# Optimization experiments

Measured on AMD Instinct MI355X. Metric: run time of the kernel, lower is better.

## Reference

```python
import jax, jax.numpy as jnp
import numpy as np

N_BOXES = 2048
N_CLASSES = 20


def _cross(a, b):
    return a[..., 0] * b[..., 1] - a[..., 1] * b[..., 0]


def _corners(box):
    # box: [5] = cx, cy, w, h, angle -> [4,2] corner coords
    cx, cy, w, h, a = box[0], box[1], box[2], box[3], box[4]
    c, s = jnp.cos(a), jnp.sin(a)
    dx = jnp.array([-1.0, 1.0, 1.0, -1.0], box.dtype) * (w * 0.5)
    dy = jnp.array([-1.0, -1.0, 1.0, 1.0], box.dtype) * (h * 0.5)
    return jnp.stack([cx + c * dx - s * dy, cy + s * dx + c * dy], axis=-1)


def _points_in_box(pts, box):
    # pts [K,2]; rotate into box frame, test axis-aligned containment
    cx, cy, w, h, a = box[0], box[1], box[2], box[3], box[4]
    c, s = jnp.cos(a), jnp.sin(a)
    px = pts[:, 0] - cx
    py = pts[:, 1] - cy
    lx = c * px + s * py
    ly = -s * px + c * py
    eps = 1e-5
    return (jnp.abs(lx) <= w * 0.5 + eps) & (jnp.abs(ly) <= h * 0.5 + eps)


def _pair_inter_area(box_a, box_b):
    # Exact convex intersection area of two rotated rectangles.
    ca = _corners(box_a)
    cb = _corners(box_b)
    # all 4x4 edge-pair intersections
    p = ca[:, None, :]
    r = (jnp.roll(ca, -1, 0) - ca)[:, None, :]
    q = cb[None, :, :]
    s_ = (jnp.roll(cb, -1, 0) - cb)[None, :, :]
    denom = _cross(r, s_)
    qp = q - p
    safe = jnp.where(jnp.abs(denom) > 1e-9, denom, 1.0)
    t = _cross(qp, s_) / safe
    u = _cross(qp, r) / safe
    valid_e = (jnp.abs(denom) > 1e-9) & (t >= 0.0) & (t <= 1.0) & (u >= 0.0) & (u <= 1.0)
    ipts = p + t[..., None] * r  # [4,4,2]
    # candidate polygon vertices: corners of A in B, corners of B in A, edge crossings
    pts = jnp.concatenate([ca, cb, ipts.reshape(16, 2)], axis=0)  # [24,2]
    mask = jnp.concatenate([_points_in_box(ca, box_b), _points_in_box(cb, box_a), valid_e.reshape(16)], axis=0)
    k = jnp.sum(mask)
    m = mask.astype(pts.dtype)[:, None]
    center = jnp.sum(pts * m, axis=0) / jnp.maximum(k, 1).astype(pts.dtype)
    d = pts - center
    ang = jnp.where(mask, jnp.arctan2(d[:, 1], d[:, 0]), 1e9)  # invalid -> sorted last
    idx = jnp.argsort(ang)
    ds = d[idx]
    ar = jnp.arange(24)
    nxt = jnp.where(ar + 1 < k, ar + 1, 0)
    cr = _cross(ds, ds[nxt])
    area = 0.5 * jnp.abs(jnp.sum(jnp.where(ar < k, cr, 0.0)))
    return jnp.where(k >= 3, area, 0.0)


def _iou_one_vs_many(box, boxes):
    inter = jax.vmap(lambda b: _pair_inter_area(box, b))(boxes)  # [N]
    area_a = box[2] * box[3]
    area_b = boxes[:, 2] * boxes[:, 3]
    return inter / (area_a + area_b - inter + 1e-9)


def _rotated_nms_mask(boxes, scores, iou_threshold):
    # sequential greedy suppression, highest score first; returns bool keep mask (original order)
    n = boxes.shape[0]
    order = jnp.argsort(-scores)
    bs = boxes[order]
    ar = jnp.arange(n)

    def body(i, keep):
        ious = _iou_one_vs_many(bs[i], bs)
        suppress = (ious > iou_threshold) & (ar > i) & keep[i]
        return keep & ~suppress

    keep_sorted = jax.lax.fori_loop(0, n, body, jnp.ones((n,), bool))
    return jnp.zeros((n,), bool).at[order].set(keep_sorted)


def setup_inputs() -> dict:
    key = jax.random.key(0)
    k1, k2, k3, k4, k5 = jax.random.split(key, 5)
    cxcy = jax.random.uniform(k1, (N_BOXES, 2), jnp.float32) * 1024.0
    wh = jax.random.uniform(k2, (N_BOXES, 2), jnp.float32) * 96.0 + 4.0
    ang = jax.random.uniform(k3, (N_BOXES, 1), jnp.float32) * np.pi
    boxes = jnp.concatenate([cxcy, wh, ang], axis=1)  # [N,5]
    scores = jax.random.uniform(k4, (N_BOXES,), jnp.float32)
    labels = jax.random.randint(k5, (N_BOXES,), 0, N_CLASSES, dtype=jnp.int64 if jax.config.read('jax_enable_x64') else jnp.int32)
    return {"boxes": boxes, "scores": scores, "labels": labels, "iou_threshold": 0.5}


def reference(boxes, scores, labels, iou_threshold):
    # multiclass NMS via coordinate-offset trick (N <= 20000 branch of forward)
    cx, cy, w, h = boxes[:, 0], boxes[:, 1], boxes[:, 2], boxes[:, 3]
    max_radius = jnp.max(jnp.sqrt(w * w + h * h)) * 0.5
    max_coord = jnp.maximum(jnp.max(cx), jnp.max(cy))
    offset_scale = (max_coord + max_radius) * 2.0 + 1.0
    offsets = labels.astype(boxes.dtype) * offset_scale
    boxes_nms = boxes.at[:, 0].add(offsets).at[:, 1].add(offsets)
    keep = _rotated_nms_mask(boxes_nms, scores, iou_threshold)
    # fixed-shape encoding of the kept-index set: score of kept boxes, 0 for suppressed
    return scores * keep.astype(scores.dtype)
```

## Files before the change

### kernel.cpp

```cpp
#include <hip/hip_runtime.h>
#include <cstdint>

typedef unsigned long long u64;
typedef uint32_t u32;

#define NB 2048
#define EDGE_CAP 16384
#define CLIST_CAP 2048


__global__ __launch_bounds__(256) void build_kernel(
    const float* __restrict__ boxes, const float* __restrict__ scores,
    const int* __restrict__ labels,
    float* __restrict__ cxp, float* __restrict__ cyp, float* __restrict__ wp,
    float* __restrict__ hp, float* __restrict__ cp, float* __restrict__ sp,
    float4* __restrict__ pxyr, float* __restrict__ sscp, int* __restrict__ sidx,
    u32* __restrict__ counters) {
#pragma clang fp contract(off)
  __shared__ float sc[NB];
  __shared__ float smc[4], smr[4];
  int t = threadIdx.x;
  if (blockIdx.x == 0 && t < 4) counters[t] = 0u;
  float mc = -1e30f, mr = -1e30f;
  for (int k = t; k < NB; k += 256) {
    float cx = boxes[k * 5 + 0];
    float cy = boxes[k * 5 + 1];
    float w = boxes[k * 5 + 2];
    float h = boxes[k * 5 + 3];
    mc = fmaxf(mc, fmaxf(cx, cy));
    float ww = w * w;
    float hh = h * h;
    mr = fmaxf(mr, sqrtf(ww + hh));
    sc[k] = scores[k];
  }
  for (int off = 32; off > 0; off >>= 1) {
    mc = fmaxf(mc, __shfl_down(mc, off));
    mr = fmaxf(mr, __shfl_down(mr, off));
  }
  if ((t & 63) == 0) { smc[t >> 6] = mc; smr[t >> 6] = mr; }
  __syncthreads();
  mc = fmaxf(fmaxf(smc[0], smc[1]), fmaxf(smc[2], smc[3]));
  mr = fmaxf(fmaxf(smr[0], smr[1]), fmaxf(smr[2], smr[3]));
  float osc = (mc + mr * 0.5f) * 2.0f + 1.0f;

  int wave = t >> 6, lane = t & 63;
  int i = blockIdx.x * 4 + wave;
  float si = sc[i];
  int rank = 0;
#pragma unroll 8
  for (int m = 0; m < NB / 64; ++m) {
    int j = m * 64 + lane;
    float sj = sc[j];
    rank += (int)((sj > si) || (sj == si && j < i));
  }
  for (int off = 32; off > 0; off >>= 1) rank += __shfl_down(rank, off);
  if (lane == 0) {
    float off = (float)labels[i] * osc;
    float cx = boxes[i * 5 + 0] + off;
    float cy = boxes[i * 5 + 1] + off;
    float w = boxes[i * 5 + 2];
    float h = boxes[i * 5 + 3];
    float a = boxes[i * 5 + 4];
    float c = cosf(a);
    float s = sinf(a);
    float ww = w * w;
    float hh = h * h;
    float rad = 0.5f * sqrtf(ww + hh);
    cxp[rank] = cx;
    cyp[rank] = cy;
    wp[rank] = w;
    hp[rank] = h;
    cp[rank] = c;
    sp[rank] = s;
    pxyr[rank] = make_float4(cx, cy, rad, 0.0f);
    sscp[rank] = si;
    sidx[rank] = i;
  }
}

__global__ __launch_bounds__(256) void candgeom_greedy_kernel(
    const float* __restrict__ cxp, const float* __restrict__ cyp,
    const float* __restrict__ wp, const float* __restrict__ hp,
    const float* __restrict__ cp, const float* __restrict__ sp,
    const float4* __restrict__ pxyr, const float* __restrict__ thrp,
    const float* __restrict__ sscp, const int* __restrict__ sidx,
    u32* __restrict__ edges, u32* __restrict__ counters,
    float* __restrict__ out) {
#pragma clang fp contract(off)
  __shared__ u32 clist[CLIST_CAP];
  __shared__ float dxL[256 * 25];
  __shared__ float dyL[256 * 25];
  __shared__ u32 ccnt;
  __shared__ int is_last;
  __shared__ u64 keepw[32];
  __shared__ u32 Sw32[64];
  __shared__ int changed;
  int t = threadIdx.x;
  if (t == 0) ccnt = 0;
  float jx[8], jy[8], jr[8];
#pragma unroll
  for (int c = 0; c < 8; ++c) {
    float4 v = pxyr[c * 256 + t];
    jx[c] = v.x; jy[c] = v.y; jr[c] = v.z;
  }
  __syncthreads();
  int i0 = blockIdx.x * 4;
#pragma unroll
  for (int di = 0; di < 4; ++di) {
    int i = i0 + di;
    float4 pi = pxyr[i];
    float ax = pi.x, ay = pi.y, ar = pi.z;
#pragma unroll
    for (int c = 0; c < 8; ++c) {
      int j = c * 256 + t;
      if (j > i) {
        float dx = jx[c] - ax, dy = jy[c] - ay;
        float rr = ar + jr[c] + 1.0f;
        if (dx * dx + dy * dy <= rr * rr) {
          u32 s = atomicAdd(&ccnt, 1u);
          if (s < CLIST_CAP) clist[s] = ((u32)i << 16) | (u32)j;
        }
      }
    }
  }
  __syncthreads();
  u32 cnt = ccnt < CLIST_CAP ? ccnt : CLIST_CAP;
  float thr = *thrp;
  float* myDx = &dxL[t * 25];
  float* myDy = &dyL[t * 25];
  for (u32 idx = t; idx < cnt; idx += 256) {
    u32 pk = clist[idx];
    int bi = (int)(pk >> 16);
    int bj = (int)(pk & 0xFFFFu);
    float acx = cxp[bi], acy = cyp[bi], aw = wp[bi], ah = hp[bi];
    float ac = cp[bi], as_ = sp[bi];
    float bcx = cxp[bj], bcy = cyp[bj], bw = wp[bj], bh = hp[bj];
    float bc = cp[bj], bs_ = sp[bj];
    const float SX[4] = {-1.f, 1.f, 1.f, -1.f};
    const float SY[4] = {-1.f, -1.f, 1.f, 1.f};
    float axx[4], ayy[4], bxx[4], byy[4];
    float ahw = aw * 0.5f, ahh = ah * 0.5f;
    float bhw = bw * 0.5f, bhh = bh * 0.5f;
#pragma unroll
    for (int q = 0; q < 4; ++q) {
      float dx = SX[q] * ahw, dy = SY[q] * ahh;
      axx[q] = acx + ac * dx - as_ * dy;
      ayy[q] = acy + as_ * dx + ac * dy;
      float ex = SX[q] * bhw, ey = SY[q] * bhh;
      bxx[q] = bcx + bc * ex - bs_ * ey;
      byy[q] = bcy + bs_ * ex + bc * ey;
    }
    float px_[24], py_[24];
    bool mk[24];
#pragma unroll
    for (int q = 0; q < 4; ++q) {
      {
        float axp = axx[q] - bcx, ayp = ayy[q] - bcy;
        float lxx = bc * axp + bs_ * ayp;
        float lyy = bc * ayp - bs_ * axp;
        mk[q] = (fabsf(lxx) <= bhw + 1e-5f) && (fabsf(lyy) <= bhh + 1e-5f);
        px_[q] = axx[q]; py_[q] = ayy[q];
      }
      {
        float axp = bxx[q] - acx, ayp = byy[q] - acy;
        float lxx = ac * axp + as_ * ayp;
        float lyy = ac * ayp - as_ * axp;
        mk[4 + q] = (fabsf(lxx) <= ahw + 1e-5f) && (fabsf(lyy) <= ahh + 1e-5f);
        px_[4 + q] = bxx[q]; py_[4 + q] = byy[q];
      }
    }
#pragma unroll
    for (int e = 0; e < 4; ++e) {
      float rx = axx[(e + 1) & 3] - axx[e];
      float ry = ayy[(e + 1) & 3] - ayy[e];
#pragma unroll
      for (int f = 0; f < 4; ++f) {
        float sx = bxx[(f + 1) & 3] - bxx[f];
        float sy = byy[(f + 1) & 3] - byy[f];
        float denom = rx * sy - ry * sx;
        float qpx = bxx[f] - axx[e];
        float qpy = byy[f] - ayy[e];
        bool dn = fabsf(denom) > 1e-9f;
        float safe = dn ? denom : 1.0f;
        float tt = (qpx * sy - qpy * sx) / safe;
        float uu = (qpx * ry - qpy * rx) / safe;
        bool valid = dn && (tt >= 0.0f) && (tt <= 1.0f) && (uu >= 0.0f) && (uu <= 1.0f);
        int id = 8 + e * 4 + f;
        px_[id] = axx[e] + tt * rx;
        py_[id] = ayy[e] + tt * ry;
        mk[id] = valid;
      }
    }
    int k = 0;
    float sx0 = 0.0f, sy0 = 0.0f;
#pragma unroll
    for (int q = 0; q < 24; ++q) {
      if (mk[q]) { k++; sx0 += px_[q]; sy0 += py_[q]; }
    }
    float kkf = (float)(k > 0 ? k : 1);
    float cxm = sx0 / kkf, cym = sy0 / kkf;
    u64 key[32];
#pragma unroll
    for (int q = 0; q < 24; ++q) {
      float dx = px_[q] - cxm, dy = py_[q] - cym;
      myDx[q] = dx; myDy[q] = dy;
      float sm = fabsf(dx) + fabsf(dy);
      float r = (sm > 0.0f) ? dy / sm : 0.0f;
      float pa;
      if (dx >= 0.0f) pa = r;
      else pa = (__float_as_uint(dy) >> 31) ? (-2.0f - r) : (2.0f - r);
      float ang = mk[q] ? pa : 1e9f;
      u32 ub = __float_as_uint(ang);
      u32 v = (ub & 0x80000000u) ? ~ub : (ub | 0x80000000u);
      key[q] = (((u64)v) << 5) | (u64)q;
    }
#pragma unroll
    for (int q = 24; q < 32; ++q) key[q] = ~0ull;
#pragma unroll
    for (int kk2 = 2; kk2 <= 32; kk2 <<= 1) {
#pragma unroll
      for (int jj = kk2 >> 1; jj > 0; jj >>= 1) {
#pragma unroll
        for (int ii = 0; ii < 32; ++ii) {
          int ll = ii ^ jj;
          if (ll > ii) {
            bool up = ((ii & kk2) == 0);
            u64 ka = key[ii], kb = key[ll];
            bool sw = up ? (ka > kb) : (ka < kb);
            key[ii] = sw ? kb : ka;
            key[ll] = sw ? ka : kb;
          }
        }
      }
    }
    float acc = 0.0f;
    int id0 = (int)(key[0] & 31ull);
    float fx = myDx[id0], fy = myDy[id0];
    float curx = fx, cury = fy;
#pragma unroll
    for (int q = 0; q < 24; ++q) {
      if (q < k - 1) {
        int idn = (int)(key[q + 1] & 31ull);
        float nx = myDx[idn], ny = myDy[idn];
        acc += curx * ny - cury * nx;
        curx = nx; cury = ny;
      } else if (q == k - 1) {
        acc += curx * fy - cury * fx;
      }
    }
    float area = 0.5f * fabsf(acc);
    float inter = (k >= 3) ? area : 0.0f;
    float areaA = aw * ah;
    float areaB = bw * bh;
    float iou = inter / (areaA + areaB - inter + 1e-9f);
    if (iou > thr) {
      u32 e = atomicAdd(&counters[1], 1u);
      if (e < EDGE_CAP) edges[e] = pk;
    }
  }
  __syncthreads();
  if (t == 0) {
    __threadfence();
    u32 old = atomicAdd(&counters[2], 1u);
    is_last = (old == (u32)(gridDim.x - 1)) ? 1 : 0;
  }
  __syncthreads();
  if (!is_last) return;
  __threadfence();
  __syncthreads();
  u32 ecnt = counters[1];
  if (ecnt > EDGE_CAP) ecnt = EDGE_CAP;
  u32 nl = ecnt < CLIST_CAP ? ecnt : CLIST_CAP;
  for (u32 k = t; k < nl; k += 256) clist[k] = edges[k];
  if (t < 32) keepw[t] = ~0ull;
  __syncthreads();
  for (int iter = 0; iter < 2060; ++iter) {
    if (t < 64) Sw32[t] = 0u;
    if (t == 0) changed = 0;
    __syncthreads();
    for (u32 k = t; k < ecnt; k += 256) {
      u32 pk = (k < CLIST_CAP) ? clist[k] : edges[k];
      int i = (int)(pk >> 16);
      int j = (int)(pk & 0xFFFFu);
      if ((keepw[i >> 6] >> (i & 63)) & 1ull)
        atomicOr(&Sw32[j >> 5], 1u << (j & 31));
    }
    __syncthreads();
    if (t < 32) {
      u64 S = ((u64)Sw32[2 * t]) | (((u64)Sw32[2 * t + 1]) << 32);
      u64 nk = ~S;
      if (nk != keepw[t]) { keepw[t] = nk; changed = 1; }
    }
    __syncthreads();
    int ch = changed;
    __syncthreads();
    if (!ch) break;
  }
  for (int p = t; p < NB; p += 256) {
    int bit = (int)((keepw[p >> 6] >> (p & 63)) & 1ull);
    out[sidx[p]] = bit ? sscp[p] : 0.0f;
  }
}

extern "C" void kernel_launch(void* const* d_in, const int* in_sizes, int n_in,
                              void* d_out, int out_size, void* d_ws, size_t ws_size,
                              hipStream_t stream) {
  const float* boxes = (const float*)d_in[0];
  const float* scores = (const float*)d_in[1];
  const int* labels = (const int*)d_in[2];
  const float* thr = (const float*)d_in[3];
  float* out = (float*)d_out;

  char* base = (char*)d_ws;
  u32* counters = (u32*)base;
  float* arr = (float*)(base + 256);
  float* cxp = arr + 0 * NB;
  float* cyp = arr + 1 * NB;
  float* wp = arr + 2 * NB;
  float* hp = arr + 3 * NB;
  float* cp = arr + 4 * NB;
  float* sp = arr + 5 * NB;
  float* sscp = arr + 6 * NB;
  int* sidx = (int*)(base + 57600);
  float4* pxyr = (float4*)(base + 66048);
  u32* edges = (u32*)(base + 102400);

  build_kernel<<<512, 256, 0, stream>>>(boxes, scores, labels, cxp, cyp, wp, hp,
                                        cp, sp, pxyr, sscp, sidx, counters);
  candgeom_greedy_kernel<<<512, 256, 0, stream>>>(cxp, cyp, wp, hp, cp, sp,
                                                  pxyr, thr, sscp, sidx,
                                                  edges, counters, out);
}
```

Measured before the change: 88.77 us.

## Fuse build and candidate/greedy kernels, drop score sort via oriented edges

Merges the two kernels into one, so boxes are no longer ranked by score and scattered into sorted SoA arrays. Each block recomputes offset centers and radii straight from the inputs, and computes cos/sin per candidate pair. Each edge is stored oriented from the higher-scored box to the lower-scored one, so the fixed-point suppression works on original indices. This removes one kernel launch, the rank pass and the intermediate global buffers. In exchange it adds a hipMemsetAsync for the counters and repeats trig and loads for every candidate pair.

```diff
diff --git a/kernel.cpp b/kernel.cpp
--- a/kernel.cpp
+++ b/kernel.cpp
@@ -9,18 +9,24 @@
 #define CLIST_CAP 2048
 
 
-__global__ __launch_bounds__(256) void build_kernel(
+__global__ __launch_bounds__(256) void nms_fused_kernel(
     const float* __restrict__ boxes, const float* __restrict__ scores,
-    const int* __restrict__ labels,
-    float* __restrict__ cxp, float* __restrict__ cyp, float* __restrict__ wp,
-    float* __restrict__ hp, float* __restrict__ cp, float* __restrict__ sp,
-    float4* __restrict__ pxyr, float* __restrict__ sscp, int* __restrict__ sidx,
-    u32* __restrict__ counters) {
+    const int* __restrict__ labels, const float* __restrict__ thrp,
+    u32* __restrict__ edges, u32* __restrict__ counters,
+    float* __restrict__ out) {
 #pragma clang fp contract(off)
   __shared__ float sc[NB];
   __shared__ float smc[4], smr[4];
+  __shared__ u32 clist[CLIST_CAP];
+  __shared__ float dxL[256 * 25];
+  __shared__ float dyL[256 * 25];
+  __shared__ u32 ccnt;
+  __shared__ int is_last;
+  __shared__ u64 keepw[32];
+  __shared__ u32 Sw32[64];
+  __shared__ int changed;
   int t = threadIdx.x;
-  if (blockIdx.x == 0 && t < 4) counters[t] = 0u;
+  if (t == 0) ccnt = 0;
   float mc = -1e30f, mr = -1e30f;
   for (int k = t; k < NB; k += 256) {
     float cx = boxes[k * 5 + 0];
@@ -43,73 +49,31 @@
   mr = fmaxf(fmaxf(smr[0], smr[1]), fmaxf(smr[2], smr[3]));
   float osc = (mc + mr * 0.5f) * 2.0f + 1.0f;
 
-  int wave = t >> 6, lane = t & 63;
-  int i = blockIdx.x * 4 + wave;
-  float si = sc[i];
-  int rank = 0;
-#pragma unroll 8
-  for (int m = 0; m < NB / 64; ++m) {
-    int j = m * 64 + lane;
-    float sj = sc[j];
-    rank += (int)((sj > si) || (sj == si && j < i));
-  }
-  for (int off = 32; off > 0; off >>= 1) rank += __shfl_down(rank, off);
-  if (lane == 0) {
-    float off = (float)labels[i] * osc;
-    float cx = boxes[i * 5 + 0] + off;
-    float cy = boxes[i * 5 + 1] + off;
-    float w = boxes[i * 5 + 2];
-    float h = boxes[i * 5 + 3];
-    float a = boxes[i * 5 + 4];
-    float c = cosf(a);
-    float s = sinf(a);
+  float jx[8], jy[8], jr[8];
+#pragma unroll
+  for (int c = 0; c < 8; ++c) {
+    int j = c * 256 + t;
+    float off = (float)labels[j] * osc;
+    float w = boxes[j * 5 + 2];
+    float h = boxes[j * 5 + 3];
     float ww = w * w;
     float hh = h * h;
-    float rad = 0.5f * sqrtf(ww + hh);
-    cxp[rank] = cx;
-    cyp[rank] = cy;
-    wp[rank] = w;
-    hp[rank] = h;
-    cp[rank] = c;
-    sp[rank] = s;
-    pxyr[rank] = make_float4(cx, cy, rad, 0.0f);
-    sscp[rank] = si;
-    sidx[rank] = i;
-  }
-}
-
-__global__ __launch_bounds__(256) void candgeom_greedy_kernel(
-    const float* __restrict__ cxp, const float* __restrict__ cyp,
-    const float* __restrict__ wp, const float* __restrict__ hp,
-    const float* __restrict__ cp, const float* __restrict__ sp,
-    const float4* __restrict__ pxyr, const float* __restrict__ thrp,
-    const float* __restrict__ sscp, const int* __restrict__ sidx,
-    u32* __restrict__ edges, u32* __restrict__ counters,
-    float* __restrict__ out) {
-#pragma clang fp contract(off)
-  __shared__ u32 clist[CLIST_CAP];
-  __shared__ float dxL[256 * 25];
-  __shared__ float dyL[256 * 25];
-  __shared__ u32 ccnt;
-  __shared__ int is_last;
-  __shared__ u64 keepw[32];
-  __shared__ u32 Sw32[64];
-  __shared__ int changed;
-  int t = threadIdx.x;
-  if (t == 0) ccnt = 0;
-  float jx[8], jy[8], jr[8];
-#pragma unroll
-  for (int c = 0; c < 8; ++c) {
-    float4 v = pxyr[c * 256 + t];
-    jx[c] = v.x; jy[c] = v.y; jr[c] = v.z;
-  }
-  __syncthreads();
+    jx[c] = boxes[j * 5 + 0] + off;
+    jy[c] = boxes[j * 5 + 1] + off;
+    jr[c] = 0.5f * sqrtf(ww + hh);
+  }
   int i0 = blockIdx.x * 4;
 #pragma unroll
   for (int di = 0; di < 4; ++di) {
     int i = i0 + di;
-    float4 pi = pxyr[i];
-    float ax = pi.x, ay = pi.y, ar = pi.z;
+    float offi = (float)labels[i] * osc;
+    float wI = boxes[i * 5 + 2];
+    float hI = boxes[i * 5 + 3];
+    float wwI = wI * wI;
+    float hhI = hI * hI;
+    float ax = boxes[i * 5 + 0] + offi;
+    float ay = boxes[i * 5 + 1] + offi;
+    float ar = 0.5f * sqrtf(wwI + hhI);
 #pragma unroll
     for (int c = 0; c < 8; ++c) {
       int j = c * 256 + t;
@@ -132,10 +96,22 @@
     u32 pk = clist[idx];
     int bi = (int)(pk >> 16);
     int bj = (int)(pk & 0xFFFFu);
-    float acx = cxp[bi], acy = cyp[bi], aw = wp[bi], ah = hp[bi];
-    float ac = cp[bi], as_ = sp[bi];
-    float bcx = cxp[bj], bcy = cyp[bj], bw = wp[bj], bh = hp[bj];
-    float bc = cp[bj], bs_ = sp[bj];
+    float offa = (float)labels[bi] * osc;
+    float acx = boxes[bi * 5 + 0] + offa;
+    float acy = boxes[bi * 5 + 1] + offa;
+    float aw = boxes[bi * 5 + 2];
+    float ah = boxes[bi * 5 + 3];
+    float aang = boxes[bi * 5 + 4];
+    float ac = cosf(aang);
+    float as_ = sinf(aang);
+    float offb = (float)labels[bj] * osc;
+    float bcx = boxes[bj * 5 + 0] + offb;
+    float bcy = boxes[bj * 5 + 1] + offb;
+    float bw = boxes[bj * 5 + 2];
+    float bh = boxes[bj * 5 + 3];
+    float bang = boxes[bj * 5 + 4];
+    float bc = cosf(bang);
+    float bs_ = sinf(bang);
     const float SX[4] = {-1.f, 1.f, 1.f, -1.f};
     const float SY[4] = {-1.f, -1.f, 1.f, 1.f};
     float axx[4], ayy[4], bxx[4], byy[4];
@@ -254,8 +230,12 @@
     float areaB = bw * bh;
     float iou = inter / (areaA + areaB - inter + 1e-9f);
     if (iou > thr) {
+      float si = sc[bi], sj2 = sc[bj];
+      bool isup = (si > sj2) || (si == sj2 && bi < bj);
+      u32 sup = isup ? (u32)bi : (u32)bj;
+      u32 sub = isup ? (u32)bj : (u32)bi;
       u32 e = atomicAdd(&counters[1], 1u);
-      if (e < EDGE_CAP) edges[e] = pk;
+      if (e < EDGE_CAP) edges[e] = (sup << 16) | sub;
     }
   }
   __syncthreads();
@@ -298,7 +278,7 @@
   }
   for (int p = t; p < NB; p += 256) {
     int bit = (int)((keepw[p >> 6] >> (p & 63)) & 1ull);
-    out[sidx[p]] = bit ? sscp[p] : 0.0f;
+    out[p] = bit ? sc[p] : 0.0f;
   }
 }
 
@@ -313,21 +293,9 @@
 
   char* base = (char*)d_ws;
   u32* counters = (u32*)base;
-  float* arr = (float*)(base + 256);
-  float* cxp = arr + 0 * NB;
-  float* cyp = arr + 1 * NB;
-  float* wp = arr + 2 * NB;
-  float* hp = arr + 3 * NB;
-  float* cp = arr + 4 * NB;
-  float* sp = arr + 5 * NB;
-  float* sscp = arr + 6 * NB;
-  int* sidx = (int*)(base + 57600);
-  float4* pxyr = (float4*)(base + 66048);
   u32* edges = (u32*)(base + 102400);
 
-  build_kernel<<<512, 256, 0, stream>>>(boxes, scores, labels, cxp, cyp, wp, hp,
-                                        cp, sp, pxyr, sscp, sidx, counters);
-  candgeom_greedy_kernel<<<512, 256, 0, stream>>>(cxp, cyp, wp, hp, cp, sp,
-                                                  pxyr, thr, sscp, sidx,
-                                                  edges, counters, out);
+  hipMemsetAsync(base, 0, 256, stream);
+  nms_fused_kernel<<<512, 256, 0, stream>>>(boxes, scores, labels, thr,
+                                            edges, counters, out);
 }
```

New measurement: 84.86 us. 1.05x faster.
